# Performance work log

Hardware: AMD Instinct MI355X
Metric: run time of the kernel (lower is better)

## Reference

```python
import jax, jax.numpy as jnp
from jax import lax
import numpy as np

B, T, D, H = 256, 512, 64, 256

def setup_inputs() -> dict:
    key = jax.random.key(0)
    ks = jax.random.split(key, 15)
    s = lambda fan_in: 1.0 / np.sqrt(fan_in)
    def lin(k, out_d, in_d):
        k1, k2 = jax.random.split(k)
        return (jax.random.uniform(k1, (out_d, in_d), jnp.float32, -s(in_d), s(in_d)),
                jax.random.uniform(k2, (out_d,), jnp.float32, -s(in_d), s(in_d)))
    W1_w, W1_b = lin(ks[0], H, D)
    U1_w, U1_b = lin(ks[1], H, H)
    W2_w, W2_b = lin(ks[2], H, H)
    U2_w, U2_b = lin(ks[3], H, H)
    o1_w, o1_b = lin(ks[4], D, H)
    o2_w, o2_b = lin(ks[5], D, H)
    g_w, g_b = lin(ks[6], H, 2 * H)
    x = jax.random.normal(ks[7], (B, T, D), jnp.float32)
    return {"x": x, "W1_w": W1_w, "W1_b": W1_b, "U1_w": U1_w, "U1_b": U1_b,
            "W2_w": W2_w, "W2_b": W2_b, "U2_w": U2_w, "U2_b": U2_b,
            "o1_w": o1_w, "o1_b": o1_b, "o2_w": o2_w, "o2_b": o2_b,
            "g_w": g_w, "g_b": g_b}


def reference(x, W1_w, W1_b, U1_w, U1_b, W2_w, W2_b, U2_w, U2_b,
              o1_w, o1_b, o2_w, o2_b, g_w, g_b):
    Bb, Tt, Dd = x.shape
    Hh = U1_w.shape[0]
    h1_0 = jnp.zeros((Bb, Hh), x.dtype)
    h2_0 = jnp.zeros((Bb, Hh), x.dtype)
    u_0 = jnp.ones((Bb, Hh), x.dtype)  # initial gate = 1 (broadcast of ones(1,1))

    def step(carry, xt):
        h1, h2, u = carry
        h1 = jnp.tanh(xt @ W1_w.T + W1_b + h1 @ U1_w.T + U1_b)
        h2_new = jnp.tanh(h1 @ W2_w.T + W2_b + h2 @ U2_w.T + U2_b)
        h2 = u * h2_new + (1.0 - u) * h2
        out = h1 @ o1_w.T + o1_b + h2 @ o2_w.T + o2_b  # (B, D)
        u = jax.nn.sigmoid(jnp.concatenate([h1, h2], axis=1) @ g_w.T + g_b)
        return (h1, h2, u), out

    _, outs = lax.scan(step, (h1_0, h2_0, u_0), jnp.swapaxes(x, 0, 1))  # (T, B, D)
    return jnp.swapaxes(outs, 0, 1)  # (B, T, D)
```

## Files before the change

### kernel.cpp

```cpp
#include <hip/hip_runtime.h>

typedef unsigned short u16;
using bf8   = __attribute__((ext_vector_type(8))) short;
using bf4   = __attribute__((ext_vector_type(4))) short;
using f32x4 = __attribute__((ext_vector_type(4))) float;

#define B_ 256
#define T_ 512
#define D_ 64
#define H_ 256
#define Tc_ 64
#define NC_ (T_ / Tc_)
#define GEMMB_ 192

#define MFMA(a, b, c) __builtin_amdgcn_mfma_f32_16x16x32_bf16(a, b, c, 0, 0, 0)

static __device__ inline u16 f2b(float f) {
    unsigned int u = __float_as_uint(f);
    unsigned int r = (u + 0x7fffu + ((u >> 16) & 1u)) >> 16;
    return (u16)r;
}
static __device__ inline float fast_tanh(float x) {
    float e = __expf(2.f * x);
    return 1.f - 2.f / (e + 1.f);
}
static __device__ inline float fast_sigmoid(float x) {
    return 1.f / (1.f + __expf(-x));
}

__global__ __launch_bounds__(256) void k_conv(
    const float* __restrict__ W1w, const float* __restrict__ U1w,
    const float* __restrict__ W2w, const float* __restrict__ U2w,
    const float* __restrict__ o1w, const float* __restrict__ o2w,
    const float* __restrict__ gw,
    u16* W1bf, u16* U1bf, u16* W2bf, u16* U2bf,
    u16* o1bf, u16* o2bf, u16* gbf)
{
    const int a = blockIdx.y;
    const float* src; u16* dst; int n;
    switch (a) {
        case 0: src = W1w; dst = W1bf; n = 16384;  break;
        case 1: src = U1w; dst = U1bf; n = 65536;  break;
        case 2: src = W2w; dst = W2bf; n = 65536;  break;
        case 3: src = U2w; dst = U2bf; n = 65536;  break;
        case 4: src = o1w; dst = o1bf; n = 16384;  break;
        case 5: src = o2w; dst = o2bf; n = 16384;  break;
        default: src = gw; dst = gbf;  n = 131072; break;
    }
    const int i = (blockIdx.x * 256 + threadIdx.x) * 4;
    if (i < n) {
        f32x4 v = *(const f32x4*)(src + i);
        bf4 o;
        o[0] = (short)f2b(v[0]); o[1] = (short)f2b(v[1]);
        o[2] = (short)f2b(v[2]); o[3] = (short)f2b(v[3]);
        *(bf4*)(dst + i) = o;
    }
}

__device__ void h1_role(
    const float* __restrict__ x, const u16* __restrict__ W1,
    const u16* __restrict__ U1, const float* __restrict__ W1b,
    const float* __restrict__ U1b, u16* __restrict__ H1,
    u16* __restrict__ h1state, int c, u16 (*buf)[H_ + 8])
{
    const int g = blockIdx.x;
    const int tid = threadIdx.x;
    const int w = tid >> 6, lane = tid & 63;
    const int col = lane & 15, quad = lane >> 4;
    const int t0 = c * Tc_;

    bf8 u1f[2][8], w1f[2][2];
    float bias[2];
#pragma unroll
    for (int i = 0; i < 2; ++i) {
        const int n = (w * 2 + i) * 16 + col;
#pragma unroll
        for (int kt = 0; kt < 8; ++kt)
            u1f[i][kt] = *(const bf8*)(U1 + (size_t)n * H_ + kt * 32 + quad * 8);
#pragma unroll
        for (int kt = 0; kt < 2; ++kt)
            w1f[i][kt] = *(const bf8*)(W1 + (size_t)n * D_ + kt * 32 + quad * 8);
        bias[i] = W1b[n] + U1b[n];
    }

    if (c == 0) {
        for (int idx = tid; idx < 16 * (H_ + 8); idx += 512)
            ((u16*)buf)[idx] = 0;
    } else {
        const int m = tid >> 5, hb = (tid & 31) * 8;
#pragma unroll
        for (int j = 0; j < 8; ++j)
            buf[m][hb + j] = h1state[(size_t)(g * 16 + m) * H_ + hb + j];
    }
    __syncthreads();

    const float* xrow = x + (size_t)(g * 16 + col) * T_ * D_ + quad * 8;
    f32x4 xa[4];
    {
        const float* xp = xrow + (size_t)t0 * D_;
        xa[0] = *(const f32x4*)xp;        xa[1] = *(const f32x4*)(xp + 4);
        xa[2] = *(const f32x4*)(xp + 32); xa[3] = *(const f32x4*)(xp + 36);
    }

    for (int tt = 0; tt < Tc_; ++tt) {
        const int tn = t0 + (tt + 1 < Tc_ ? tt + 1 : tt);
        f32x4 xan[4];
        {
            const float* xp = xrow + (size_t)tn * D_;
            xan[0] = *(const f32x4*)xp;        xan[1] = *(const f32x4*)(xp + 4);
            xan[2] = *(const f32x4*)(xp + 32); xan[3] = *(const f32x4*)(xp + 36);
        }
        bf8 haf[8];
#pragma unroll
        for (int kt = 0; kt < 8; ++kt)
            haf[kt] = *(const bf8*)&buf[col][kt * 32 + quad * 8];
        __syncthreads();

        bf8 xaf[2];
#pragma unroll
        for (int kt = 0; kt < 2; ++kt) {
            bf8 v;
#pragma unroll
            for (int j = 0; j < 4; ++j) {
                v[j]     = (short)f2b(xa[kt * 2][j]);
                v[j + 4] = (short)f2b(xa[kt * 2 + 1][j]);
            }
            xaf[kt] = v;
        }

        f32x4 acc[2];
#pragma unroll
        for (int i = 0; i < 2; ++i) {
            acc[i][0] = bias[i]; acc[i][1] = bias[i];
            acc[i][2] = bias[i]; acc[i][3] = bias[i];
        }
#pragma unroll
        for (int kt = 0; kt < 8; ++kt)
#pragma unroll
            for (int i = 0; i < 2; ++i)
                acc[i] = MFMA(haf[kt], u1f[i][kt], acc[i]);
#pragma unroll
        for (int kt = 0; kt < 2; ++kt)
#pragma unroll
            for (int i = 0; i < 2; ++i)
                acc[i] = MFMA(xaf[kt], w1f[i][kt], acc[i]);

#pragma unroll
        for (int i = 0; i < 2; ++i) {
            const int n = (w * 2 + i) * 16 + col;
#pragma unroll
            for (int r = 0; r < 4; ++r)
                buf[quad * 4 + r][n] = f2b(fast_tanh(acc[i][r]));
        }
        __syncthreads();
        {
            const int m = tid >> 5, hb = (tid & 31) * 8;
            bf8 v0 = *(const bf8*)&buf[m][hb];
            u16* dst = H1 + ((size_t)tt * 256 + g * 16 + m) * H_ + hb;
            *(bf8*)dst = v0;
        }
        xa[0] = xan[0]; xa[1] = xan[1]; xa[2] = xan[2]; xa[3] = xan[3];
    }
    __syncthreads();
    {
        const int m = tid >> 5, hb = (tid & 31) * 8;
#pragma unroll
        for (int j = 0; j < 8; ++j)
            h1state[(size_t)(g * 16 + m) * H_ + hb + j] = buf[m][hb + j];
    }
}

__device__ void h2_role(
    const u16* __restrict__ U2, const u16* __restrict__ gw,
    const u16* __restrict__ o2w,
    const float* __restrict__ W2c, const float* __restrict__ G1c,
    const float* __restrict__ O1c,
    float* __restrict__ out, float* __restrict__ h2state,
    float* __restrict__ ustate, int ch, u16 (*buf)[H_ + 8])
{
    const int g = blockIdx.x - 16;
    const int tid = threadIdx.x;
    const int w = tid >> 6, lane = tid & 63;
    const int col = lane & 15, quad = lane >> 4;
    const int t0 = ch * Tc_;

    bf8 u2f[2][8], g2f[2][8], o2f[8];
#pragma unroll
    for (int i = 0; i < 2; ++i) {
        const int n = (w * 2 + i) * 16 + col;
#pragma unroll
        for (int kt = 0; kt < 8; ++kt) {
            u2f[i][kt] = *(const bf8*)(U2 + (size_t)n * H_ + kt * 32 + quad * 8);
            g2f[i][kt] = *(const bf8*)(gw + (size_t)n * (2 * H_) + H_ + kt * 32 + quad * 8);
        }
    }
    if (w < 4) {
#pragma unroll
        for (int kt = 0; kt < 8; ++kt)
            o2f[kt] = *(const bf8*)(o2w + (size_t)(w * 16 + col) * H_ + kt * 32 + quad * 8);
    }

    f32x4 h2p[2], up[2];
    if (ch == 0) {
#pragma unroll
        for (int i = 0; i < 2; ++i) {
            h2p[i][0]=0.f; h2p[i][1]=0.f; h2p[i][2]=0.f; h2p[i][3]=0.f;
            up[i][0]=1.f;  up[i][1]=1.f;  up[i][2]=1.f;  up[i][3]=1.f;
        }
    } else {
#pragma unroll
        for (int i = 0; i < 2; ++i) {
            size_t idx = (((size_t)g * 16 + (w * 2 + i)) * 64 + lane) * 4;
            h2p[i] = *(const f32x4*)(h2state + idx);
            up[i]  = *(const f32x4*)(ustate + idx);
        }
    }

#pragma unroll
    for (int i = 0; i < 2; ++i) {
        const int n = (w * 2 + i) * 16 + col;
#pragma unroll
        for (int r = 0; r < 4; ++r) buf[quad * 4 + r][n] = f2b(h2p[i][r]);
    }
    __syncthreads();
    bf8 h2af[8];
#pragma unroll
    for (int kt = 0; kt < 8; ++kt)
        h2af[kt] = *(const bf8*)&buf[col][kt * 32 + quad * 8];
    __syncthreads();

    f32x4 w2cr[2];
#pragma unroll
    for (int i = 0; i < 2; ++i)
        w2cr[i] = *(const f32x4*)(W2c +
            ((((size_t)g * Tc_ + 0) * 16 + (w * 2 + i)) * 64 + lane) * 4);

    for (int tt = 0; tt < Tc_; ++tt) {
        const int ttn = (tt + 1 < Tc_) ? tt + 1 : tt;
        f32x4 w2cn[2], g1cc[2], o1cc;
#pragma unroll
        for (int i = 0; i < 2; ++i) {
            w2cn[i] = *(const f32x4*)(W2c +
                ((((size_t)g * Tc_ + ttn) * 16 + (w * 2 + i)) * 64 + lane) * 4);
            g1cc[i] = *(const f32x4*)(G1c +
                ((((size_t)g * Tc_ + tt) * 16 + (w * 2 + i)) * 64 + lane) * 4);
        }
        if (w < 4)
            o1cc = *(const f32x4*)(O1c +
                ((((size_t)g * Tc_ + tt) * 4 + w) * 64 + lane) * 4);

        f32x4 acc1[2];
#pragma unroll
        for (int i = 0; i < 2; ++i) acc1[i] = w2cr[i];
#pragma unroll
        for (int kt = 0; kt < 8; ++kt)
#pragma unroll
            for (int i = 0; i < 2; ++i)
                acc1[i] = MFMA(h2af[kt], u2f[i][kt], acc1[i]);

#pragma unroll
        for (int i = 0; i < 2; ++i)
#pragma unroll
            for (int r = 0; r < 4; ++r) {
                float h2n = fast_tanh(acc1[i][r]);
                h2p[i][r] = up[i][r] * h2n + (1.f - up[i][r]) * h2p[i][r];
            }
#pragma unroll
        for (int i = 0; i < 2; ++i) {
            const int n = (w * 2 + i) * 16 + col;
#pragma unroll
            for (int r = 0; r < 4; ++r) buf[quad * 4 + r][n] = f2b(h2p[i][r]);
        }
        __syncthreads();
#pragma unroll
        for (int kt = 0; kt < 8; ++kt)
            h2af[kt] = *(const bf8*)&buf[col][kt * 32 + quad * 8];
        __syncthreads();

        f32x4 accg[2], acco;
#pragma unroll
        for (int i = 0; i < 2; ++i) accg[i] = g1cc[i];
        if (w < 4) {
            acco = o1cc;
#pragma unroll
            for (int kt = 0; kt < 8; ++kt) {
                acco = MFMA(h2af[kt], o2f[kt], acco);
#pragma unroll
                for (int i = 0; i < 2; ++i)
                    accg[i] = MFMA(h2af[kt], g2f[i][kt], accg[i]);
            }
            const int t = t0 + tt;
#pragma unroll
            for (int r = 0; r < 4; ++r)
                out[((size_t)(g * 16 + quad * 4 + r) * T_ + t) * D_ + w * 16 + col] =
                    acco[r];
        } else {
#pragma unroll
            for (int kt = 0; kt < 8; ++kt)
#pragma unroll
                for (int i = 0; i < 2; ++i)
                    accg[i] = MFMA(h2af[kt], g2f[i][kt], accg[i]);
        }
#pragma unroll
        for (int i = 0; i < 2; ++i)
#pragma unroll
            for (int r = 0; r < 4; ++r) up[i][r] = fast_sigmoid(accg[i][r]);

#pragma unroll
        for (int i = 0; i < 2; ++i) w2cr[i] = w2cn[i];
    }
#pragma unroll
    for (int i = 0; i < 2; ++i) {
        size_t idx = (((size_t)g * 16 + (w * 2 + i)) * 64 + lane) * 4;
        *(f32x4*)(h2state + idx) = h2p[i];
        *(f32x4*)(ustate + idx)  = up[i];
    }
}

__global__ __launch_bounds__(512, 2) void k_pipe(
    const float* __restrict__ x, const u16* __restrict__ W1,
    const u16* __restrict__ U1, const float* __restrict__ W1b,
    const float* __restrict__ U1b, u16* __restrict__ H1w,
    u16* __restrict__ h1state,
    const u16* __restrict__ U2, const u16* __restrict__ gwgt,
    const u16* __restrict__ o2w,
    const float* __restrict__ W2cr, const float* __restrict__ G1cr,
    const float* __restrict__ O1cr,
    float* __restrict__ out, float* __restrict__ h2state,
    float* __restrict__ ustate,
    const u16* __restrict__ H1r, const u16* __restrict__ W2,
    const u16* __restrict__ o1w,
    const float* __restrict__ W2b, const float* __restrict__ U2b,
    const float* __restrict__ gbias, const float* __restrict__ o1b,
    const float* __restrict__ o2b,
    float* __restrict__ W2cw, float* __restrict__ G1cw, float* __restrict__ O1cw,
    int c)
{
    __shared__ __align__(16) u16 buf[16][H_ + 8];
    if (blockIdx.x < 16) {
        if (c < NC_)
            h1_role(x, W1, U1, W1b, U1b, H1w, h1state, c, buf);
    } else if (blockIdx.x < 32) {
        if (c >= 2)
            h2_role(U2, gwgt, o2w, W2cr, G1cr, O1cr, out, h2state, ustate, c - 2, buf);
    } else {
        if (c >= 1 && c <= NC_) {
            const int gbk = blockIdx.x - 32;
            const int tid = threadIdx.x;
            const int w = tid >> 6, lane = tid & 63;
            const int col = lane & 15, quad = lane >> 4;
            const int Wv = gbk * 8 + w;
            const int NT = (Tc_ * 256 / 16) * 9;

            for (int task = Wv; task < NT; task += GEMMB_ * 8) {
                const int mt = task & 1023, ny = task >> 10;
                const int mrow = mt * 16;

                f32x4 acc[4];
#pragma unroll
                for (int i = 0; i < 4; ++i) { acc[i][0]=0.f; acc[i][1]=0.f; acc[i][2]=0.f; acc[i][3]=0.f; }

#pragma unroll
                for (int kt = 0; kt < 8; ++kt) {
                    const int k = kt * 32 + quad * 8;
                    bf8 af = *(const bf8*)(H1r + (size_t)(mrow + col) * H_ + k);
#pragma unroll
                    for (int i = 0; i < 4; ++i) {
                        const int n = ny * 64 + i * 16 + col;
                        const u16* bp;
                        if (n < 256)      bp = W2   + (size_t)n * H_ + k;
                        else if (n < 512) bp = gwgt + (size_t)(n - 256) * (2 * H_) + k;
                        else              bp = o1w  + (size_t)(n - 512) * H_ + k;
                        bf8 bfv = *(const bf8*)bp;
                        acc[i] = MFMA(af, bfv, acc[i]);
                    }
                }

                const int tt = mrow >> 8;
                const int g  = (mrow & 255) >> 4;
#pragma unroll
                for (int i = 0; i < 4; ++i) {
                    const int n = ny * 64 + i * 16 + col;
                    float bias;
                    if (n < 256)      bias = W2b[n] + U2b[n];
                    else if (n < 512) bias = gbias[n - 256];
                    else              bias = o1b[n - 512] + o2b[n - 512];
                    f32x4 v;
#pragma unroll
                    for (int r = 0; r < 4; ++r) v[r] = acc[i][r] + bias;
                    const int nt = ny * 4 + i;
                    if (nt < 16) {
                        size_t idx = ((((size_t)g * Tc_ + tt) * 16 + nt) * 64 + lane) * 4;
                        *(f32x4*)(W2cw + idx) = v;
                    } else if (nt < 32) {
                        size_t idx = ((((size_t)g * Tc_ + tt) * 16 + (nt - 16)) * 64 + lane) * 4;
                        *(f32x4*)(G1cw + idx) = v;
                    } else {
                        size_t idx = ((((size_t)g * Tc_ + tt) * 4 + (nt - 32)) * 64 + lane) * 4;
                        *(f32x4*)(O1cw + idx) = v;
                    }
                }
            }
        }
    }
}

extern "C" void kernel_launch(void* const* d_in, const int* in_sizes, int n_in,
                              void* d_out, int out_size, void* d_ws, size_t ws_size,
                              hipStream_t stream)
{
    const float* x   = (const float*)d_in[0];
    const float* W1w = (const float*)d_in[1];
    const float* W1b = (const float*)d_in[2];
    const float* U1w = (const float*)d_in[3];
    const float* U1b = (const float*)d_in[4];
    const float* W2w = (const float*)d_in[5];
    const float* W2b = (const float*)d_in[6];
    const float* U2w = (const float*)d_in[7];
    const float* U2b = (const float*)d_in[8];
    const float* o1w = (const float*)d_in[9];
    const float* o1b = (const float*)d_in[10];
    const float* o2w = (const float*)d_in[11];
    const float* o2b = (const float*)d_in[12];
    const float* gw  = (const float*)d_in[13];
    const float* gb  = (const float*)d_in[14];
    float* out = (float*)d_out;
    (void)in_sizes; (void)n_in; (void)out_size; (void)ws_size;

    char* p = (char*)d_ws;
    u16* W1bf = (u16*)p; p += 16384 * 2;
    u16* U1bf = (u16*)p; p += 65536 * 2;
    u16* W2bf = (u16*)p; p += 65536 * 2;
    u16* U2bf = (u16*)p; p += 65536 * 2;
    u16* o1bf = (u16*)p; p += 16384 * 2;
    u16* o2bf = (u16*)p; p += 16384 * 2;
    u16* gbf  = (u16*)p; p += 131072 * 2;
    u16* H1[2]; float* W2c[2]; float* G1c[2]; float* O1c[2];
    for (int pa = 0; pa < 2; ++pa) {
        H1[pa]  = (u16*)p;   p += (size_t)Tc_ * 131072;
        W2c[pa] = (float*)p; p += (size_t)Tc_ * 262144;
        G1c[pa] = (float*)p; p += (size_t)Tc_ * 262144;
        O1c[pa] = (float*)p; p += (size_t)Tc_ * 65536;
    }
    u16* h1s   = (u16*)p;  p += 131072;
    float* h2s = (float*)p; p += 262144;
    float* us  = (float*)p;

    k_conv<<<dim3(128, 7), 256, 0, stream>>>(W1w, U1w, W2w, U2w, o1w, o2w, gw,
                                             W1bf, U1bf, W2bf, U2bf, o1bf, o2bf, gbf);

    for (int c = 0; c <= NC_ + 1; ++c) {
        const int pw = c & 1;
        const int pg = (c + 1) & 1;
        const int ph = c & 1;
        k_pipe<<<32 + GEMMB_, 512, 0, stream>>>(
            x, W1bf, U1bf, W1b, U1b, H1[pw], h1s,
            U2bf, gbf, o2bf, W2c[ph], G1c[ph], O1c[ph],
            out, h2s, us,
            H1[pg], W2bf, o1bf, W2b, U2b, gb, o1b, o2b,
            W2c[pg], G1c[pg], O1c[pg], c);
    }
}
```

Baseline: 1.323 ms.

## Split h2 recurrence into producer/gate warp groups and pre-convert x to bf16

The h2 role is split into two warp groups. Four warps compute the U2 tanh path and four compute the gate and output projections. The gate projection lags by one step and the u and h2 state are exchanged through LDS, so the two matmul chains can run concurrently within a step instead of sequentially. Separately, x is converted to bf16 once in the conversion kernel, removing per-step f32-to-bf16 conversion in the h1 loop. The cost is an extra full pass over x, more LDS, and an extra sync per step.

```diff
diff --git a/kernel.cpp b/kernel.cpp
--- a/kernel.cpp
+++ b/kernel.cpp
@@ -32,20 +32,21 @@
     const float* __restrict__ W1w, const float* __restrict__ U1w,
     const float* __restrict__ W2w, const float* __restrict__ U2w,
     const float* __restrict__ o1w, const float* __restrict__ o2w,
-    const float* __restrict__ gw,
+    const float* __restrict__ gw,  const float* __restrict__ x,
     u16* W1bf, u16* U1bf, u16* W2bf, u16* U2bf,
-    u16* o1bf, u16* o2bf, u16* gbf)
+    u16* o1bf, u16* o2bf, u16* gbf, u16* xbf)
 {
     const int a = blockIdx.y;
     const float* src; u16* dst; int n;
     switch (a) {
-        case 0: src = W1w; dst = W1bf; n = 16384;  break;
-        case 1: src = U1w; dst = U1bf; n = 65536;  break;
-        case 2: src = W2w; dst = W2bf; n = 65536;  break;
-        case 3: src = U2w; dst = U2bf; n = 65536;  break;
-        case 4: src = o1w; dst = o1bf; n = 16384;  break;
-        case 5: src = o2w; dst = o2bf; n = 16384;  break;
-        default: src = gw; dst = gbf;  n = 131072; break;
+        case 0: src = W1w; dst = W1bf; n = 16384;   break;
+        case 1: src = U1w; dst = U1bf; n = 65536;   break;
+        case 2: src = W2w; dst = W2bf; n = 65536;   break;
+        case 3: src = U2w; dst = U2bf; n = 65536;   break;
+        case 4: src = o1w; dst = o1bf; n = 16384;   break;
+        case 5: src = o2w; dst = o2bf; n = 16384;   break;
+        case 6: src = gw;  dst = gbf;  n = 131072;  break;
+        default: src = x;  dst = xbf;  n = 8388608; break;
     }
     const int i = (blockIdx.x * 256 + threadIdx.x) * 4;
     if (i < n) {
@@ -58,7 +59,7 @@
 }
 
 __device__ void h1_role(
-    const float* __restrict__ x, const u16* __restrict__ W1,
+    const u16* __restrict__ xbf, const u16* __restrict__ W1,
     const u16* __restrict__ U1, const float* __restrict__ W1b,
     const float* __restrict__ U1b, u16* __restrict__ H1,
     u16* __restrict__ h1state, int c, u16 (*buf)[H_ + 8])
@@ -94,40 +95,22 @@
     }
     __syncthreads();
 
-    const float* xrow = x + (size_t)(g * 16 + col) * T_ * D_ + quad * 8;
-    f32x4 xa[4];
-    {
-        const float* xp = xrow + (size_t)t0 * D_;
-        xa[0] = *(const f32x4*)xp;        xa[1] = *(const f32x4*)(xp + 4);
-        xa[2] = *(const f32x4*)(xp + 32); xa[3] = *(const f32x4*)(xp + 36);
-    }
-
+    const u16* xrow = xbf + (size_t)(g * 16 + col) * T_ * D_ + quad * 8;
+    bf8 xa0 = *(const bf8*)(xrow + (size_t)t0 * D_);
+    bf8 xa1 = *(const bf8*)(xrow + (size_t)t0 * D_ + 32);
+
+#pragma unroll 1
     for (int tt = 0; tt < Tc_; ++tt) {
         const int tn = t0 + (tt + 1 < Tc_ ? tt + 1 : tt);
-        f32x4 xan[4];
-        {
-            const float* xp = xrow + (size_t)tn * D_;
-            xan[0] = *(const f32x4*)xp;        xan[1] = *(const f32x4*)(xp + 4);
-            xan[2] = *(const f32x4*)(xp + 32); xan[3] = *(const f32x4*)(xp + 36);
-        }
+        bf8 xn0 = *(const bf8*)(xrow + (size_t)tn * D_);
+        bf8 xn1 = *(const bf8*)(xrow + (size_t)tn * D_ + 32);
+
         bf8 haf[8];
 #pragma unroll
         for (int kt = 0; kt < 8; ++kt)
             haf[kt] = *(const bf8*)&buf[col][kt * 32 + quad * 8];
         __syncthreads();
 
-        bf8 xaf[2];
-#pragma unroll
-        for (int kt = 0; kt < 2; ++kt) {
-            bf8 v;
-#pragma unroll
-            for (int j = 0; j < 4; ++j) {
-                v[j]     = (short)f2b(xa[kt * 2][j]);
-                v[j + 4] = (short)f2b(xa[kt * 2 + 1][j]);
-            }
-            xaf[kt] = v;
-        }
-
         f32x4 acc[2];
 #pragma unroll
         for (int i = 0; i < 2; ++i) {
@@ -140,10 +123,10 @@
             for (int i = 0; i < 2; ++i)
                 acc[i] = MFMA(haf[kt], u1f[i][kt], acc[i]);
 #pragma unroll
-        for (int kt = 0; kt < 2; ++kt)
-#pragma unroll
-            for (int i = 0; i < 2; ++i)
-                acc[i] = MFMA(xaf[kt], w1f[i][kt], acc[i]);
+        for (int i = 0; i < 2; ++i) {
+            acc[i] = MFMA(xa0, w1f[i][0], acc[i]);
+            acc[i] = MFMA(xa1, w1f[i][1], acc[i]);
+        }
 
 #pragma unroll
         for (int i = 0; i < 2; ++i) {
@@ -159,7 +142,7 @@
             u16* dst = H1 + ((size_t)tt * 256 + g * 16 + m) * H_ + hb;
             *(bf8*)dst = v0;
         }
-        xa[0] = xan[0]; xa[1] = xan[1]; xa[2] = xan[2]; xa[3] = xan[3];
+        xa0 = xn0; xa1 = xn1;
     }
     __syncthreads();
     {
@@ -176,149 +159,197 @@
     const float* __restrict__ W2c, const float* __restrict__ G1c,
     const float* __restrict__ O1c,
     float* __restrict__ out, float* __restrict__ h2state,
-    float* __restrict__ ustate, int ch, u16 (*buf)[H_ + 8])
+    float* __restrict__ ustate, int ch,
+    u16 (*h2buf)[H_ + 8], float* u_lds, float* h2f32)
 {
     const int g = blockIdx.x - 16;
     const int tid = threadIdx.x;
     const int w = tid >> 6, lane = tid & 63;
     const int col = lane & 15, quad = lane >> 4;
     const int t0 = ch * Tc_;
-
-    bf8 u2f[2][8], g2f[2][8], o2f[8];
-#pragma unroll
-    for (int i = 0; i < 2; ++i) {
-        const int n = (w * 2 + i) * 16 + col;
-#pragma unroll
-        for (int kt = 0; kt < 8; ++kt) {
-            u2f[i][kt] = *(const bf8*)(U2 + (size_t)n * H_ + kt * 32 + quad * 8);
-            g2f[i][kt] = *(const bf8*)(gw + (size_t)n * (2 * H_) + H_ + kt * 32 + quad * 8);
-        }
-    }
-    if (w < 4) {
+    const bool isP = (w < 4);
+    const int wp = w & 3;
+
+    bf8 wf[4][8];
+    bf8 o2f[8];
+    if (isP) {
+#pragma unroll
+        for (int i = 0; i < 4; ++i)
+#pragma unroll
+            for (int kt = 0; kt < 8; ++kt)
+                wf[i][kt] = *(const bf8*)(U2 + (size_t)((wp * 4 + i) * 16 + col) * H_ +
+                                          kt * 32 + quad * 8);
+    } else {
+#pragma unroll
+        for (int i = 0; i < 4; ++i)
+#pragma unroll
+            for (int kt = 0; kt < 8; ++kt)
+                wf[i][kt] = *(const bf8*)(gw + (size_t)((wp * 4 + i) * 16 + col) * (2 * H_) +
+                                          H_ + kt * 32 + quad * 8);
 #pragma unroll
         for (int kt = 0; kt < 8; ++kt)
-            o2f[kt] = *(const bf8*)(o2w + (size_t)(w * 16 + col) * H_ + kt * 32 + quad * 8);
-    }
-
-    f32x4 h2p[2], up[2];
-    if (ch == 0) {
-#pragma unroll
-        for (int i = 0; i < 2; ++i) {
-            h2p[i][0]=0.f; h2p[i][1]=0.f; h2p[i][2]=0.f; h2p[i][3]=0.f;
-            up[i][0]=1.f;  up[i][1]=1.f;  up[i][2]=1.f;  up[i][3]=1.f;
-        }
+            o2f[kt] = *(const bf8*)(o2w + (size_t)(wp * 16 + col) * H_ + kt * 32 + quad * 8);
+    }
+
+    if (isP) {
+        f32x4 h2p[4];
+        if (ch == 0) {
+#pragma unroll
+            for (int i = 0; i < 4; ++i) {
+                h2p[i][0] = 0.f; h2p[i][1] = 0.f; h2p[i][2] = 0.f; h2p[i][3] = 0.f;
+            }
+        } else {
+#pragma unroll
+            for (int i = 0; i < 4; ++i)
+                h2p[i] = *(const f32x4*)(h2state +
+                    (((size_t)g * 16 + (wp * 4 + i)) * 64 + lane) * 4);
+        }
+#pragma unroll
+        for (int i = 0; i < 4; ++i) {
+            *(f32x4*)(h2f32 + ((wp * 4 + i) * 64 + lane) * 4) = h2p[i];
+            const int n = wp * 64 + i * 16 + col;
+#pragma unroll
+            for (int r = 0; r < 4; ++r)
+                h2buf[quad * 4 + r][n] = f2b(h2p[i][r]);
+        }
+    }
+    __syncthreads();
+
+    f32x4 w2cn[4];
+    f32x4 g1cn[4], o1cn;
+    if (isP) {
+#pragma unroll
+        for (int i = 0; i < 4; ++i)
+            w2cn[i] = *(const f32x4*)(W2c +
+                ((((size_t)g * Tc_) * 16 + (wp * 4 + i)) * 64 + lane) * 4);
     } else {
 #pragma unroll
-        for (int i = 0; i < 2; ++i) {
-            size_t idx = (((size_t)g * 16 + (w * 2 + i)) * 64 + lane) * 4;
-            h2p[i] = *(const f32x4*)(h2state + idx);
-            up[i]  = *(const f32x4*)(ustate + idx);
-        }
-    }
-
-#pragma unroll
-    for (int i = 0; i < 2; ++i) {
-        const int n = (w * 2 + i) * 16 + col;
-#pragma unroll
-        for (int r = 0; r < 4; ++r) buf[quad * 4 + r][n] = f2b(h2p[i][r]);
-    }
-    __syncthreads();
-    bf8 h2af[8];
-#pragma unroll
-    for (int kt = 0; kt < 8; ++kt)
-        h2af[kt] = *(const bf8*)&buf[col][kt * 32 + quad * 8];
-    __syncthreads();
-
-    f32x4 w2cr[2];
-#pragma unroll
-    for (int i = 0; i < 2; ++i)
-        w2cr[i] = *(const f32x4*)(W2c +
-            ((((size_t)g * Tc_ + 0) * 16 + (w * 2 + i)) * 64 + lane) * 4);
-
-    for (int tt = 0; tt < Tc_; ++tt) {
-        const int ttn = (tt + 1 < Tc_) ? tt + 1 : tt;
-        f32x4 w2cn[2], g1cc[2], o1cc;
-#pragma unroll
-        for (int i = 0; i < 2; ++i) {
-            w2cn[i] = *(const f32x4*)(W2c +
-                ((((size_t)g * Tc_ + ttn) * 16 + (w * 2 + i)) * 64 + lane) * 4);
-            g1cc[i] = *(const f32x4*)(G1c +
-                ((((size_t)g * Tc_ + tt) * 16 + (w * 2 + i)) * 64 + lane) * 4);
-        }
-        if (w < 4)
-            o1cc = *(const f32x4*)(O1c +
-                ((((size_t)g * Tc_ + tt) * 4 + w) * 64 + lane) * 4);
-
-        f32x4 acc1[2];
-#pragma unroll
-        for (int i = 0; i < 2; ++i) acc1[i] = w2cr[i];
-#pragma unroll
-        for (int kt = 0; kt < 8; ++kt)
-#pragma unroll
-            for (int i = 0; i < 2; ++i)
-                acc1[i] = MFMA(h2af[kt], u2f[i][kt], acc1[i]);
-
-#pragma unroll
-        for (int i = 0; i < 2; ++i)
-#pragma unroll
-            for (int r = 0; r < 4; ++r) {
-                float h2n = fast_tanh(acc1[i][r]);
-                h2p[i][r] = up[i][r] * h2n + (1.f - up[i][r]) * h2p[i][r];
-            }
-#pragma unroll
-        for (int i = 0; i < 2; ++i) {
-            const int n = (w * 2 + i) * 16 + col;
-#pragma unroll
-            for (int r = 0; r < 4; ++r) buf[quad * 4 + r][n] = f2b(h2p[i][r]);
-        }
-        __syncthreads();
-#pragma unroll
-        for (int kt = 0; kt < 8; ++kt)
-            h2af[kt] = *(const bf8*)&buf[col][kt * 32 + quad * 8];
-        __syncthreads();
-
-        f32x4 accg[2], acco;
-#pragma unroll
-        for (int i = 0; i < 2; ++i) accg[i] = g1cc[i];
-        if (w < 4) {
-            acco = o1cc;
+        for (int i = 0; i < 4; ++i)
+            g1cn[i] = *(const f32x4*)(G1c +
+                ((((size_t)g * Tc_) * 16 + (wp * 4 + i)) * 64 + lane) * 4);
+        o1cn = *(const f32x4*)(O1c + ((((size_t)g * Tc_) * 4 + wp) * 64 + lane) * 4);
+    }
+
+#pragma unroll 1
+    for (int tt = 0; tt <= Tc_; ++tt) {
+        f32x4 th[4];
+        if (isP) {
+            if (tt < Tc_) {
+                bf8 h2af[8];
+#pragma unroll
+                for (int kt = 0; kt < 8; ++kt)
+                    h2af[kt] = *(const bf8*)&h2buf[col][kt * 32 + quad * 8];
+                f32x4 acc[4];
+#pragma unroll
+                for (int i = 0; i < 4; ++i) acc[i] = w2cn[i];
+                const int tpf = (tt + 1 < Tc_) ? tt + 1 : Tc_ - 1;
+#pragma unroll
+                for (int i = 0; i < 4; ++i)
+                    w2cn[i] = *(const f32x4*)(W2c +
+                        ((((size_t)g * Tc_ + tpf) * 16 + (wp * 4 + i)) * 64 + lane) * 4);
+#pragma unroll
+                for (int kt = 0; kt < 8; ++kt)
+#pragma unroll
+                    for (int i = 0; i < 4; ++i)
+                        acc[i] = MFMA(h2af[kt], wf[i][kt], acc[i]);
+#pragma unroll
+                for (int i = 0; i < 4; ++i)
+#pragma unroll
+                    for (int r = 0; r < 4; ++r)
+                        th[i][r] = fast_tanh(acc[i][r]);
+            }
+        } else if (tt >= 1) {
+            bf8 h2af[8];
+#pragma unroll
+            for (int kt = 0; kt < 8; ++kt)
+                h2af[kt] = *(const bf8*)&h2buf[col][kt * 32 + quad * 8];
+            f32x4 accg[4], acco = o1cn;
+#pragma unroll
+            for (int i = 0; i < 4; ++i) accg[i] = g1cn[i];
+            const int tpf = (tt < Tc_) ? tt : Tc_ - 1;
+#pragma unroll
+            for (int i = 0; i < 4; ++i)
+                g1cn[i] = *(const f32x4*)(G1c +
+                    ((((size_t)g * Tc_ + tpf) * 16 + (wp * 4 + i)) * 64 + lane) * 4);
+            o1cn = *(const f32x4*)(O1c +
+                ((((size_t)g * Tc_ + tpf) * 4 + wp) * 64 + lane) * 4);
 #pragma unroll
             for (int kt = 0; kt < 8; ++kt) {
                 acco = MFMA(h2af[kt], o2f[kt], acco);
 #pragma unroll
-                for (int i = 0; i < 2; ++i)
-                    accg[i] = MFMA(h2af[kt], g2f[i][kt], accg[i]);
-            }
-            const int t = t0 + tt;
+                for (int i = 0; i < 4; ++i)
+                    accg[i] = MFMA(h2af[kt], wf[i][kt], accg[i]);
+            }
+            const int t = t0 + tt - 1;
 #pragma unroll
             for (int r = 0; r < 4; ++r)
-                out[((size_t)(g * 16 + quad * 4 + r) * T_ + t) * D_ + w * 16 + col] =
+                out[((size_t)(g * 16 + quad * 4 + r) * T_ + t) * D_ + wp * 16 + col] =
                     acco[r];
-        } else {
-#pragma unroll
-            for (int kt = 0; kt < 8; ++kt)
-#pragma unroll
-                for (int i = 0; i < 2; ++i)
-                    accg[i] = MFMA(h2af[kt], g2f[i][kt], accg[i]);
-        }
-#pragma unroll
-        for (int i = 0; i < 2; ++i)
-#pragma unroll
-            for (int r = 0; r < 4; ++r) up[i][r] = fast_sigmoid(accg[i][r]);
-
-#pragma unroll
-        for (int i = 0; i < 2; ++i) w2cr[i] = w2cn[i];
-    }
-#pragma unroll
-    for (int i = 0; i < 2; ++i) {
-        size_t idx = (((size_t)g * 16 + (w * 2 + i)) * 64 + lane) * 4;
-        *(f32x4*)(h2state + idx) = h2p[i];
-        *(f32x4*)(ustate + idx)  = up[i];
+#pragma unroll
+            for (int i = 0; i < 4; ++i)
+#pragma unroll
+                for (int r = 0; r < 4; ++r)
+                    accg[i][r] = fast_sigmoid(accg[i][r]);
+            if (tt < Tc_) {
+#pragma unroll
+                for (int i = 0; i < 4; ++i)
+                    *(f32x4*)(u_lds + ((wp * 4 + i) * 64 + lane) * 4) = accg[i];
+            } else {
+#pragma unroll
+                for (int i = 0; i < 4; ++i)
+                    *(f32x4*)(ustate +
+                        (((size_t)g * 16 + (wp * 4 + i)) * 64 + lane) * 4) = accg[i];
+            }
+        }
+        __syncthreads();
+        if (isP && tt < Tc_) {
+            f32x4 uu[4], h2o[4];
+            if (tt == 0) {
+                if (ch == 0) {
+#pragma unroll
+                    for (int i = 0; i < 4; ++i) {
+                        uu[i][0] = 1.f; uu[i][1] = 1.f; uu[i][2] = 1.f; uu[i][3] = 1.f;
+                    }
+                } else {
+#pragma unroll
+                    for (int i = 0; i < 4; ++i)
+                        uu[i] = *(const f32x4*)(ustate +
+                            (((size_t)g * 16 + (wp * 4 + i)) * 64 + lane) * 4);
+                }
+            } else {
+#pragma unroll
+                for (int i = 0; i < 4; ++i)
+                    uu[i] = *(const f32x4*)(u_lds + ((wp * 4 + i) * 64 + lane) * 4);
+            }
+#pragma unroll
+            for (int i = 0; i < 4; ++i)
+                h2o[i] = *(const f32x4*)(h2f32 + ((wp * 4 + i) * 64 + lane) * 4);
+#pragma unroll
+            for (int i = 0; i < 4; ++i)
+#pragma unroll
+                for (int r = 0; r < 4; ++r)
+                    h2o[i][r] = uu[i][r] * th[i][r] + (1.f - uu[i][r]) * h2o[i][r];
+#pragma unroll
+            for (int i = 0; i < 4; ++i) {
+                *(f32x4*)(h2f32 + ((wp * 4 + i) * 64 + lane) * 4) = h2o[i];
+                const int n = wp * 64 + i * 16 + col;
+#pragma unroll
+                for (int r = 0; r < 4; ++r)
+                    h2buf[quad * 4 + r][n] = f2b(h2o[i][r]);
+            }
+        }
+        __syncthreads();
+    }
+    if (isP) {
+#pragma unroll
+        for (int i = 0; i < 4; ++i)
+            *(f32x4*)(h2state + (((size_t)g * 16 + (wp * 4 + i)) * 64 + lane) * 4) =
+                *(const f32x4*)(h2f32 + ((wp * 4 + i) * 64 + lane) * 4);
     }
 }
 
 __global__ __launch_bounds__(512, 2) void k_pipe(
-    const float* __restrict__ x, const u16* __restrict__ W1,
+    const u16* __restrict__ xbf, const u16* __restrict__ W1,
     const u16* __restrict__ U1, const float* __restrict__ W1b,
     const float* __restrict__ U1b, u16* __restrict__ H1w,
     u16* __restrict__ h1state,
@@ -336,13 +367,16 @@
     float* __restrict__ W2cw, float* __restrict__ G1cw, float* __restrict__ O1cw,
     int c)
 {
-    __shared__ __align__(16) u16 buf[16][H_ + 8];
+    __shared__ __align__(16) u16 h2buf[16][H_ + 8];
+    __shared__ __align__(16) float u_lds[4096];
+    __shared__ __align__(16) float h2f32[4096];
     if (blockIdx.x < 16) {
         if (c < NC_)
-            h1_role(x, W1, U1, W1b, U1b, H1w, h1state, c, buf);
+            h1_role(xbf, W1, U1, W1b, U1b, H1w, h1state, c, h2buf);
     } else if (blockIdx.x < 32) {
         if (c >= 2)
-            h2_role(U2, gwgt, o2w, W2cr, G1cr, O1cr, out, h2state, ustate, c - 2, buf);
+            h2_role(U2, gwgt, o2w, W2cr, G1cr, O1cr, out, h2state, ustate, c - 2,
+                    h2buf, u_lds, h2f32);
     } else {
         if (c >= 1 && c <= NC_) {
             const int gbk = blockIdx.x - 32;
@@ -435,6 +469,7 @@
     u16* o1bf = (u16*)p; p += 16384 * 2;
     u16* o2bf = (u16*)p; p += 16384 * 2;
     u16* gbf  = (u16*)p; p += 131072 * 2;
+    u16* xbf  = (u16*)p; p += (size_t)8388608 * 2;
     u16* H1[2]; float* W2c[2]; float* G1c[2]; float* O1c[2];
     for (int pa = 0; pa < 2; ++pa) {
         H1[pa]  = (u16*)p;   p += (size_t)Tc_ * 131072;
@@ -446,15 +481,16 @@
     float* h2s = (float*)p; p += 262144;
     float* us  = (float*)p;
 
-    k_conv<<<dim3(128, 7), 256, 0, stream>>>(W1w, U1w, W2w, U2w, o1w, o2w, gw,
-                                             W1bf, U1bf, W2bf, U2bf, o1bf, o2bf, gbf);
+    k_conv<<<dim3(8192, 8), 256, 0, stream>>>(W1w, U1w, W2w, U2w, o1w, o2w, gw, x,
+                                              W1bf, U1bf, W2bf, U2bf, o1bf, o2bf,
+                                              gbf, xbf);
 
     for (int c = 0; c <= NC_ + 1; ++c) {
         const int pw = c & 1;
         const int pg = (c + 1) & 1;
         const int ph = c & 1;
         k_pipe<<<32 + GEMMB_, 512, 0, stream>>>(
-            x, W1bf, U1bf, W1b, U1b, H1[pw], h1s,
+            xbf, W1bf, U1bf, W1b, U1b, H1[pw], h1s,
             U2bf, gbf, o2bf, W2c[ph], G1c[ph], O1c[ph],
             out, h2s, us,
             H1[pg], W2bf, o1bf, W2b, U2b, gb, o1b, o2b,
```

New measurement: 1.681 ms. 1.27x slower.

## Split h2 recurrence to 8-row blocks, skew gate/U2 steps, store precomputes in bf16

Applied to the files above, without the earlier changes.

The h2 recurrence now uses 32 blocks, each covering 8 batch rows (the upper MFMA rows are zero-padded). Each step is software-skewed so that the gate and output MFMAs for step t-1 share one h2 fragment load and one barrier with the U2 MFMA for step t. The precomputed W2/gate/output projections are written and read as bf16 instead of fp32, which halves their traffic. x is pre-converted to bf16 in the conversion kernel, and the GEMM block count is raised so the grid stays filled. The costs are half-wasted MFMA rows in the h2 role, an extra full-x conversion pass, and some precision loss from storing the projections in bf16.

```diff
diff --git a/kernel.cpp b/kernel.cpp
--- a/kernel.cpp
+++ b/kernel.cpp
@@ -11,7 +11,7 @@
 #define H_ 256
 #define Tc_ 64
 #define NC_ (T_ / Tc_)
-#define GEMMB_ 192
+#define GEMMB_ 208
 
 #define MFMA(a, b, c) __builtin_amdgcn_mfma_f32_16x16x32_bf16(a, b, c, 0, 0, 0)
 
@@ -20,6 +20,15 @@
     unsigned int r = (u + 0x7fffu + ((u >> 16) & 1u)) >> 16;
     return (u16)r;
 }
+static __device__ inline float b2f(u16 u) {
+    return __uint_as_float(((unsigned int)u) << 16);
+}
+static __device__ inline f32x4 b4x(bf4 v) {
+    f32x4 r;
+    r[0] = b2f((u16)v[0]); r[1] = b2f((u16)v[1]);
+    r[2] = b2f((u16)v[2]); r[3] = b2f((u16)v[3]);
+    return r;
+}
 static __device__ inline float fast_tanh(float x) {
     float e = __expf(2.f * x);
     return 1.f - 2.f / (e + 1.f);
@@ -32,20 +41,21 @@
     const float* __restrict__ W1w, const float* __restrict__ U1w,
     const float* __restrict__ W2w, const float* __restrict__ U2w,
     const float* __restrict__ o1w, const float* __restrict__ o2w,
-    const float* __restrict__ gw,
+    const float* __restrict__ gw,  const float* __restrict__ x,
     u16* W1bf, u16* U1bf, u16* W2bf, u16* U2bf,
-    u16* o1bf, u16* o2bf, u16* gbf)
+    u16* o1bf, u16* o2bf, u16* gbf, u16* xbf)
 {
     const int a = blockIdx.y;
     const float* src; u16* dst; int n;
     switch (a) {
-        case 0: src = W1w; dst = W1bf; n = 16384;  break;
-        case 1: src = U1w; dst = U1bf; n = 65536;  break;
-        case 2: src = W2w; dst = W2bf; n = 65536;  break;
-        case 3: src = U2w; dst = U2bf; n = 65536;  break;
-        case 4: src = o1w; dst = o1bf; n = 16384;  break;
-        case 5: src = o2w; dst = o2bf; n = 16384;  break;
-        default: src = gw; dst = gbf;  n = 131072; break;
+        case 0: src = W1w; dst = W1bf; n = 16384;   break;
+        case 1: src = U1w; dst = U1bf; n = 65536;   break;
+        case 2: src = W2w; dst = W2bf; n = 65536;   break;
+        case 3: src = U2w; dst = U2bf; n = 65536;   break;
+        case 4: src = o1w; dst = o1bf; n = 16384;   break;
+        case 5: src = o2w; dst = o2bf; n = 16384;   break;
+        case 6: src = gw;  dst = gbf;  n = 131072;  break;
+        default: src = x;  dst = xbf;  n = 8388608; break;
     }
     const int i = (blockIdx.x * 256 + threadIdx.x) * 4;
     if (i < n) {
@@ -58,7 +68,7 @@
 }
 
 __device__ void h1_role(
-    const float* __restrict__ x, const u16* __restrict__ W1,
+    const u16* __restrict__ xbf, const u16* __restrict__ W1,
     const u16* __restrict__ U1, const float* __restrict__ W1b,
     const float* __restrict__ U1b, u16* __restrict__ H1,
     u16* __restrict__ h1state, int c, u16 (*buf)[H_ + 8])
@@ -94,40 +104,22 @@
     }
     __syncthreads();
 
-    const float* xrow = x + (size_t)(g * 16 + col) * T_ * D_ + quad * 8;
-    f32x4 xa[4];
-    {
-        const float* xp = xrow + (size_t)t0 * D_;
-        xa[0] = *(const f32x4*)xp;        xa[1] = *(const f32x4*)(xp + 4);
-        xa[2] = *(const f32x4*)(xp + 32); xa[3] = *(const f32x4*)(xp + 36);
-    }
-
+    const u16* xrow = xbf + (size_t)(g * 16 + col) * T_ * D_ + quad * 8;
+    bf8 xa0 = *(const bf8*)(xrow + (size_t)t0 * D_);
+    bf8 xa1 = *(const bf8*)(xrow + (size_t)t0 * D_ + 32);
+
+#pragma unroll 1
     for (int tt = 0; tt < Tc_; ++tt) {
         const int tn = t0 + (tt + 1 < Tc_ ? tt + 1 : tt);
-        f32x4 xan[4];
-        {
-            const float* xp = xrow + (size_t)tn * D_;
-            xan[0] = *(const f32x4*)xp;        xan[1] = *(const f32x4*)(xp + 4);
-            xan[2] = *(const f32x4*)(xp + 32); xan[3] = *(const f32x4*)(xp + 36);
-        }
+        bf8 xn0 = *(const bf8*)(xrow + (size_t)tn * D_);
+        bf8 xn1 = *(const bf8*)(xrow + (size_t)tn * D_ + 32);
+
         bf8 haf[8];
 #pragma unroll
         for (int kt = 0; kt < 8; ++kt)
             haf[kt] = *(const bf8*)&buf[col][kt * 32 + quad * 8];
         __syncthreads();
 
-        bf8 xaf[2];
-#pragma unroll
-        for (int kt = 0; kt < 2; ++kt) {
-            bf8 v;
-#pragma unroll
-            for (int j = 0; j < 4; ++j) {
-                v[j]     = (short)f2b(xa[kt * 2][j]);
-                v[j + 4] = (short)f2b(xa[kt * 2 + 1][j]);
-            }
-            xaf[kt] = v;
-        }
-
         f32x4 acc[2];
 #pragma unroll
         for (int i = 0; i < 2; ++i) {
@@ -140,10 +132,10 @@
             for (int i = 0; i < 2; ++i)
                 acc[i] = MFMA(haf[kt], u1f[i][kt], acc[i]);
 #pragma unroll
-        for (int kt = 0; kt < 2; ++kt)
-#pragma unroll
-            for (int i = 0; i < 2; ++i)
-                acc[i] = MFMA(xaf[kt], w1f[i][kt], acc[i]);
+        for (int i = 0; i < 2; ++i) {
+            acc[i] = MFMA(xa0, w1f[i][0], acc[i]);
+            acc[i] = MFMA(xa1, w1f[i][1], acc[i]);
+        }
 
 #pragma unroll
         for (int i = 0; i < 2; ++i) {
@@ -159,7 +151,7 @@
             u16* dst = H1 + ((size_t)tt * 256 + g * 16 + m) * H_ + hb;
             *(bf8*)dst = v0;
         }
-        xa[0] = xan[0]; xa[1] = xan[1]; xa[2] = xan[2]; xa[3] = xan[3];
+        xa0 = xn0; xa1 = xn1;
     }
     __syncthreads();
     {
@@ -173,15 +165,17 @@
 __device__ void h2_role(
     const u16* __restrict__ U2, const u16* __restrict__ gw,
     const u16* __restrict__ o2w,
-    const float* __restrict__ W2c, const float* __restrict__ G1c,
-    const float* __restrict__ O1c,
+    const u16* __restrict__ W2c, const u16* __restrict__ G1c,
+    const u16* __restrict__ O1c,
     float* __restrict__ out, float* __restrict__ h2state,
     float* __restrict__ ustate, int ch, u16 (*buf)[H_ + 8])
 {
-    const int g = blockIdx.x - 16;
+    const int g8 = blockIdx.x - 16;
     const int tid = threadIdx.x;
     const int w = tid >> 6, lane = tid & 63;
     const int col = lane & 15, quad = lane >> 4;
+    const int lane32 = lane & 31;
+    const bool low = (quad < 2);
     const int t0 = ch * Tc_;
 
     bf8 u2f[2][8], g2f[2][8], o2f[8];
@@ -200,132 +194,179 @@
             o2f[kt] = *(const bf8*)(o2w + (size_t)(w * 16 + col) * H_ + kt * 32 + quad * 8);
     }
 
-    f32x4 h2p[2], up[2];
-    if (ch == 0) {
-#pragma unroll
-        for (int i = 0; i < 2; ++i) {
-            h2p[i][0]=0.f; h2p[i][1]=0.f; h2p[i][2]=0.f; h2p[i][3]=0.f;
-            up[i][0]=1.f;  up[i][1]=1.f;  up[i][2]=1.f;  up[i][3]=1.f;
-        }
-    } else {
-#pragma unroll
-        for (int i = 0; i < 2; ++i) {
-            size_t idx = (((size_t)g * 16 + (w * 2 + i)) * 64 + lane) * 4;
+    f32x4 h2p[2], uu[2];
+#pragma unroll
+    for (int i = 0; i < 2; ++i) {
+        h2p[i][0]=0.f; h2p[i][1]=0.f; h2p[i][2]=0.f; h2p[i][3]=0.f;
+        uu[i][0]=1.f;  uu[i][1]=1.f;  uu[i][2]=1.f;  uu[i][3]=1.f;
+    }
+    if (ch > 0 && low) {
+#pragma unroll
+        for (int i = 0; i < 2; ++i) {
+            size_t idx = (((size_t)g8 * 16 + (w * 2 + i)) * 32 + lane32) * 4;
             h2p[i] = *(const f32x4*)(h2state + idx);
-            up[i]  = *(const f32x4*)(ustate + idx);
-        }
-    }
-
-#pragma unroll
-    for (int i = 0; i < 2; ++i) {
-        const int n = (w * 2 + i) * 16 + col;
-#pragma unroll
-        for (int r = 0; r < 4; ++r) buf[quad * 4 + r][n] = f2b(h2p[i][r]);
-    }
+            uu[i]  = *(const f32x4*)(ustate + idx);
+        }
+    }
+
+    for (int idx = tid; idx < 16 * (H_ + 8); idx += 512)
+        ((u16*)buf)[idx] = 0;
     __syncthreads();
-    bf8 h2af[8];
-#pragma unroll
-    for (int kt = 0; kt < 8; ++kt)
-        h2af[kt] = *(const bf8*)&buf[col][kt * 32 + quad * 8];
+    if (low) {
+#pragma unroll
+        for (int i = 0; i < 2; ++i) {
+            const int n = (w * 2 + i) * 16 + col;
+#pragma unroll
+            for (int r = 0; r < 4; ++r)
+                buf[quad * 4 + r][n] = f2b(h2p[i][r]);
+        }
+    }
     __syncthreads();
 
-    f32x4 w2cr[2];
-#pragma unroll
-    for (int i = 0; i < 2; ++i)
-        w2cr[i] = *(const f32x4*)(W2c +
-            ((((size_t)g * Tc_ + 0) * 16 + (w * 2 + i)) * 64 + lane) * 4);
-
-    for (int tt = 0; tt < Tc_; ++tt) {
-        const int ttn = (tt + 1 < Tc_) ? tt + 1 : tt;
-        f32x4 w2cn[2], g1cc[2], o1cc;
-#pragma unroll
-        for (int i = 0; i < 2; ++i) {
-            w2cn[i] = *(const f32x4*)(W2c +
-                ((((size_t)g * Tc_ + ttn) * 16 + (w * 2 + i)) * 64 + lane) * 4);
-            g1cc[i] = *(const f32x4*)(G1c +
-                ((((size_t)g * Tc_ + tt) * 16 + (w * 2 + i)) * 64 + lane) * 4);
-        }
-        if (w < 4)
-            o1cc = *(const f32x4*)(O1c +
-                ((((size_t)g * Tc_ + tt) * 4 + w) * 64 + lane) * 4);
-
-        f32x4 acc1[2];
-#pragma unroll
-        for (int i = 0; i < 2; ++i) acc1[i] = w2cr[i];
-#pragma unroll
-        for (int kt = 0; kt < 8; ++kt)
-#pragma unroll
-            for (int i = 0; i < 2; ++i)
-                acc1[i] = MFMA(h2af[kt], u2f[i][kt], acc1[i]);
-
+    bf4 w2n[2], g1n[2], o1n;
+    if (low) {
 #pragma unroll
         for (int i = 0; i < 2; ++i)
-#pragma unroll
-            for (int r = 0; r < 4; ++r) {
-                float h2n = fast_tanh(acc1[i][r]);
-                h2p[i][r] = up[i][r] * h2n + (1.f - up[i][r]) * h2p[i][r];
-            }
-#pragma unroll
-        for (int i = 0; i < 2; ++i) {
-            const int n = (w * 2 + i) * 16 + col;
-#pragma unroll
-            for (int r = 0; r < 4; ++r) buf[quad * 4 + r][n] = f2b(h2p[i][r]);
-        }
-        __syncthreads();
+            w2n[i] = *(const bf4*)(W2c +
+                ((((size_t)g8 * Tc_) * 16 + (w * 2 + i)) * 32 + lane32) * 4);
+    }
+
+#pragma unroll 1
+    for (int tt = 0; tt <= Tc_; ++tt) {
+        bf8 h2af[8];
 #pragma unroll
         for (int kt = 0; kt < 8; ++kt)
             h2af[kt] = *(const bf8*)&buf[col][kt * 32 + quad * 8];
         __syncthreads();
 
-        f32x4 accg[2], acco;
-#pragma unroll
-        for (int i = 0; i < 2; ++i) accg[i] = g1cc[i];
-        if (w < 4) {
-            acco = o1cc;
-#pragma unroll
-            for (int kt = 0; kt < 8; ++kt) {
-                acco = MFMA(h2af[kt], o2f[kt], acco);
+        f32x4 accU[2], accG[2], accO;
+#pragma unroll
+        for (int i = 0; i < 2; ++i) {
+            accU[i][0]=0.f; accU[i][1]=0.f; accU[i][2]=0.f; accU[i][3]=0.f;
+            accG[i][0]=0.f; accG[i][1]=0.f; accG[i][2]=0.f; accG[i][3]=0.f;
+        }
+        accO[0]=0.f; accO[1]=0.f; accO[2]=0.f; accO[3]=0.f;
+
+        if (tt < Tc_ && low) {
+#pragma unroll
+            for (int i = 0; i < 2; ++i) accU[i] = b4x(w2n[i]);
+        }
+        if (tt >= 1 && low) {
+#pragma unroll
+            for (int i = 0; i < 2; ++i) accG[i] = b4x(g1n[i]);
+            if (w < 4) accO = b4x(o1n);
+        }
+        if (tt < Tc_ && low) {
+            const int tpf = (tt + 1 < Tc_) ? tt + 1 : Tc_ - 1;
+#pragma unroll
+            for (int i = 0; i < 2; ++i) {
+                w2n[i] = *(const bf4*)(W2c +
+                    ((((size_t)g8 * Tc_ + tpf) * 16 + (w * 2 + i)) * 32 + lane32) * 4);
+                g1n[i] = *(const bf4*)(G1c +
+                    ((((size_t)g8 * Tc_ + tt) * 16 + (w * 2 + i)) * 32 + lane32) * 4);
+            }
+            if (w < 4)
+                o1n = *(const bf4*)(O1c +
+                    ((((size_t)g8 * Tc_ + tt) * 4 + w) * 32 + lane32) * 4);
+        }
+
+        if (tt == 0) {
+#pragma unroll
+            for (int kt = 0; kt < 8; ++kt)
 #pragma unroll
                 for (int i = 0; i < 2; ++i)
-                    accg[i] = MFMA(h2af[kt], g2f[i][kt], accg[i]);
+                    accU[i] = MFMA(h2af[kt], u2f[i][kt], accU[i]);
+        } else if (tt < Tc_) {
+            if (w < 4) {
+#pragma unroll
+                for (int kt = 0; kt < 8; ++kt) {
+                    accO = MFMA(h2af[kt], o2f[kt], accO);
+#pragma unroll
+                    for (int i = 0; i < 2; ++i) {
+                        accU[i] = MFMA(h2af[kt], u2f[i][kt], accU[i]);
+                        accG[i] = MFMA(h2af[kt], g2f[i][kt], accG[i]);
+                    }
+                }
+            } else {
+#pragma unroll
+                for (int kt = 0; kt < 8; ++kt)
+#pragma unroll
+                    for (int i = 0; i < 2; ++i) {
+                        accU[i] = MFMA(h2af[kt], u2f[i][kt], accU[i]);
+                        accG[i] = MFMA(h2af[kt], g2f[i][kt], accG[i]);
+                    }
             }
-            const int t = t0 + tt;
-#pragma unroll
-            for (int r = 0; r < 4; ++r)
-                out[((size_t)(g * 16 + quad * 4 + r) * T_ + t) * D_ + w * 16 + col] =
-                    acco[r];
         } else {
-#pragma unroll
-            for (int kt = 0; kt < 8; ++kt)
-#pragma unroll
-                for (int i = 0; i < 2; ++i)
-                    accg[i] = MFMA(h2af[kt], g2f[i][kt], accg[i]);
-        }
-#pragma unroll
-        for (int i = 0; i < 2; ++i)
-#pragma unroll
-            for (int r = 0; r < 4; ++r) up[i][r] = fast_sigmoid(accg[i][r]);
-
-#pragma unroll
-        for (int i = 0; i < 2; ++i) w2cr[i] = w2cn[i];
-    }
-#pragma unroll
-    for (int i = 0; i < 2; ++i) {
-        size_t idx = (((size_t)g * 16 + (w * 2 + i)) * 64 + lane) * 4;
-        *(f32x4*)(h2state + idx) = h2p[i];
-        *(f32x4*)(ustate + idx)  = up[i];
+            if (w < 4) {
+#pragma unroll
+                for (int kt = 0; kt < 8; ++kt) {
+                    accO = MFMA(h2af[kt], o2f[kt], accO);
+#pragma unroll
+                    for (int i = 0; i < 2; ++i)
+                        accG[i] = MFMA(h2af[kt], g2f[i][kt], accG[i]);
+                }
+            } else {
+#pragma unroll
+                for (int kt = 0; kt < 8; ++kt)
+#pragma unroll
+                    for (int i = 0; i < 2; ++i)
+                        accG[i] = MFMA(h2af[kt], g2f[i][kt], accG[i]);
+            }
+        }
+
+        if (tt >= 1) {
+            if (w < 4 && low) {
+                const int t = t0 + tt - 1;
+#pragma unroll
+                for (int r = 0; r < 4; ++r)
+                    out[((size_t)(g8 * 8 + quad * 4 + r) * T_ + t) * D_ + w * 16 + col] =
+                        accO[r];
+            }
+#pragma unroll
+            for (int i = 0; i < 2; ++i)
+#pragma unroll
+                for (int r = 0; r < 4; ++r)
+                    uu[i][r] = fast_sigmoid(accG[i][r]);
+        }
+        if (tt < Tc_) {
+#pragma unroll
+            for (int i = 0; i < 2; ++i)
+#pragma unroll
+                for (int r = 0; r < 4; ++r) {
+                    float h2n = fast_tanh(accU[i][r]);
+                    h2p[i][r] = uu[i][r] * h2n + (1.f - uu[i][r]) * h2p[i][r];
+                }
+            if (low) {
+#pragma unroll
+                for (int i = 0; i < 2; ++i) {
+                    const int n = (w * 2 + i) * 16 + col;
+#pragma unroll
+                    for (int r = 0; r < 4; ++r)
+                        buf[quad * 4 + r][n] = f2b(h2p[i][r]);
+                }
+            }
+        }
+        __syncthreads();
+    }
+    if (low) {
+#pragma unroll
+        for (int i = 0; i < 2; ++i) {
+            size_t idx = (((size_t)g8 * 16 + (w * 2 + i)) * 32 + lane32) * 4;
+            *(f32x4*)(h2state + idx) = h2p[i];
+            *(f32x4*)(ustate + idx)  = uu[i];
+        }
     }
 }
 
 __global__ __launch_bounds__(512, 2) void k_pipe(
-    const float* __restrict__ x, const u16* __restrict__ W1,
+    const u16* __restrict__ xbf, const u16* __restrict__ W1,
     const u16* __restrict__ U1, const float* __restrict__ W1b,
     const float* __restrict__ U1b, u16* __restrict__ H1w,
     u16* __restrict__ h1state,
     const u16* __restrict__ U2, const u16* __restrict__ gwgt,
     const u16* __restrict__ o2w,
-    const float* __restrict__ W2cr, const float* __restrict__ G1cr,
-    const float* __restrict__ O1cr,
+    const u16* __restrict__ W2cr, const u16* __restrict__ G1cr,
+    const u16* __restrict__ O1cr,
     float* __restrict__ out, float* __restrict__ h2state,
     float* __restrict__ ustate,
     const u16* __restrict__ H1r, const u16* __restrict__ W2,
@@ -333,19 +374,19 @@
     const float* __restrict__ W2b, const float* __restrict__ U2b,
     const float* __restrict__ gbias, const float* __restrict__ o1b,
     const float* __restrict__ o2b,
-    float* __restrict__ W2cw, float* __restrict__ G1cw, float* __restrict__ O1cw,
+    u16* __restrict__ W2cw, u16* __restrict__ G1cw, u16* __restrict__ O1cw,
     int c)
 {
     __shared__ __align__(16) u16 buf[16][H_ + 8];
     if (blockIdx.x < 16) {
         if (c < NC_)
-            h1_role(x, W1, U1, W1b, U1b, H1w, h1state, c, buf);
-    } else if (blockIdx.x < 32) {
+            h1_role(xbf, W1, U1, W1b, U1b, H1w, h1state, c, buf);
+    } else if (blockIdx.x < 48) {
         if (c >= 2)
             h2_role(U2, gwgt, o2w, W2cr, G1cr, O1cr, out, h2state, ustate, c - 2, buf);
     } else {
         if (c >= 1 && c <= NC_) {
-            const int gbk = blockIdx.x - 32;
+            const int gbk = blockIdx.x - 48;
             const int tid = threadIdx.x;
             const int w = tid >> 6, lane = tid & 63;
             const int col = lane & 15, quad = lane >> 4;
@@ -376,8 +417,10 @@
                     }
                 }
 
-                const int tt = mrow >> 8;
-                const int g  = (mrow & 255) >> 4;
+                const int tt  = mrow >> 8;
+                const int g16 = (mrow & 255) >> 4;
+                const int g8  = g16 * 2 + (quad >> 1);
+                const int sub = ((quad & 1) << 4) | col;
 #pragma unroll
                 for (int i = 0; i < 4; ++i) {
                     const int n = ny * 64 + i * 16 + col;
@@ -385,20 +428,18 @@
                     if (n < 256)      bias = W2b[n] + U2b[n];
                     else if (n < 512) bias = gbias[n - 256];
                     else              bias = o1b[n - 512] + o2b[n - 512];
-                    f32x4 v;
-#pragma unroll
-                    for (int r = 0; r < 4; ++r) v[r] = acc[i][r] + bias;
+                    bf4 v;
+#pragma unroll
+                    for (int r = 0; r < 4; ++r) v[r] = (short)f2b(acc[i][r] + bias);
                     const int nt = ny * 4 + i;
-                    if (nt < 16) {
-                        size_t idx = ((((size_t)g * Tc_ + tt) * 16 + nt) * 64 + lane) * 4;
-                        *(f32x4*)(W2cw + idx) = v;
-                    } else if (nt < 32) {
-                        size_t idx = ((((size_t)g * Tc_ + tt) * 16 + (nt - 16)) * 64 + lane) * 4;
-                        *(f32x4*)(G1cw + idx) = v;
-                    } else {
-                        size_t idx = ((((size_t)g * Tc_ + tt) * 4 + (nt - 32)) * 64 + lane) * 4;
-                        *(f32x4*)(O1cw + idx) = v;
-                    }
+                    u16* dst;
+                    if (nt < 16)
+                        dst = W2cw + ((((size_t)g8 * Tc_ + tt) * 16 + nt) * 32 + sub) * 4;
+                    else if (nt < 32)
+                        dst = G1cw + ((((size_t)g8 * Tc_ + tt) * 16 + (nt - 16)) * 32 + sub) * 4;
+                    else
+                        dst = O1cw + ((((size_t)g8 * Tc_ + tt) * 4 + (nt - 32)) * 32 + sub) * 4;
+                    *(bf4*)dst = v;
                 }
             }
         }
@@ -435,26 +476,28 @@
     u16* o1bf = (u16*)p; p += 16384 * 2;
     u16* o2bf = (u16*)p; p += 16384 * 2;
     u16* gbf  = (u16*)p; p += 131072 * 2;
-    u16* H1[2]; float* W2c[2]; float* G1c[2]; float* O1c[2];
+    u16* xbf  = (u16*)p; p += (size_t)8388608 * 2;
+    u16* H1[2]; u16* W2c[2]; u16* G1c[2]; u16* O1c[2];
     for (int pa = 0; pa < 2; ++pa) {
-        H1[pa]  = (u16*)p;   p += (size_t)Tc_ * 131072;
-        W2c[pa] = (float*)p; p += (size_t)Tc_ * 262144;
-        G1c[pa] = (float*)p; p += (size_t)Tc_ * 262144;
-        O1c[pa] = (float*)p; p += (size_t)Tc_ * 65536;
+        H1[pa]  = (u16*)p; p += (size_t)Tc_ * 131072;
+        W2c[pa] = (u16*)p; p += (size_t)Tc_ * 131072;
+        G1c[pa] = (u16*)p; p += (size_t)Tc_ * 131072;
+        O1c[pa] = (u16*)p; p += (size_t)Tc_ * 32768;
     }
     u16* h1s   = (u16*)p;  p += 131072;
     float* h2s = (float*)p; p += 262144;
     float* us  = (float*)p;
 
-    k_conv<<<dim3(128, 7), 256, 0, stream>>>(W1w, U1w, W2w, U2w, o1w, o2w, gw,
-                                             W1bf, U1bf, W2bf, U2bf, o1bf, o2bf, gbf);
+    k_conv<<<dim3(8192, 8), 256, 0, stream>>>(W1w, U1w, W2w, U2w, o1w, o2w, gw, x,
+                                              W1bf, U1bf, W2bf, U2bf, o1bf, o2bf,
+                                              gbf, xbf);
 
     for (int c = 0; c <= NC_ + 1; ++c) {
         const int pw = c & 1;
         const int pg = (c + 1) & 1;
         const int ph = c & 1;
-        k_pipe<<<32 + GEMMB_, 512, 0, stream>>>(
-            x, W1bf, U1bf, W1b, U1b, H1[pw], h1s,
+        k_pipe<<<48 + GEMMB_, 512, 0, stream>>>(
+            xbf, W1bf, U1bf, W1b, U1b, H1[pw], h1s,
             U2bf, gbf, o2bf, W2c[ph], G1c[ph], O1c[ph],
             out, h2s, us,
             H1[pg], W2bf, o1bf, W2b, U2b, gb, o1b, o2b,
```

Measured after the change: 1.733 ms. +31.0%, slower.
